# Kernel tuning notes

Hardware: AMD Instinct MI355X
Metric: run time of the kernel (lower is better)

Reference implementation:

```python
import jax, jax.numpy as jnp
import numpy as np

H = 16
D_MODEL = 1024
D_K = D_MODEL // H
NEG = -1e9


def setup_inputs() -> dict:
    key = jax.random.key(0)
    ks = jax.random.split(key, 12)
    B, S = 2, 2048
    inp = {
        "query": jax.random.normal(ks[0], (B, S, D_MODEL), jnp.float32),
        "key": jax.random.normal(ks[1], (B, S, D_MODEL), jnp.float32),
        "value": jax.random.normal(ks[2], (B, S, D_MODEL), jnp.float32),
        "mask": jnp.ones((B, 1, S), jnp.int32),
    }
    s = 1.0 / np.sqrt(D_MODEL)
    for i, nm in enumerate(["Wq", "Wk", "Wv", "Wo"]):
        inp[nm] = jax.random.normal(ks[3 + i], (D_MODEL, D_MODEL), jnp.float32) * s
        inp["b" + nm[1]] = jax.random.normal(ks[7 + i], (D_MODEL,), jnp.float32) * s
    return inp


def _split_heads(x):
    B, S, _ = x.shape
    return x.reshape(B, S, H, D_K).transpose(0, 2, 1, 3)  # [B,H,S,Dk]


def reference(query, key, value, mask, Wq, bq, Wk, bk, Wv, bv, Wo, bo):
    q = _split_heads(query @ Wq + bq)
    k = _split_heads(key @ Wk + bk)
    v = _split_heads(value @ Wv + bv)
    scores = jnp.einsum("bhqd,bhkd->bhqk", q, k) / jnp.sqrt(jnp.float32(D_K))
    # mask [B,1,Sk] -> broadcast as [B,1,1,Sk]
    scores = jnp.where(mask[:, None, :, :] == 0, NEG, scores)
    attn = jax.nn.softmax(scores, axis=-1)  # dropout is identity in eval mode
    out = jnp.einsum("bhqk,bhkd->bhqd", attn, v)
    B, _, Sq, _ = out.shape
    out = out.transpose(0, 2, 1, 3).reshape(B, Sq, H * D_K)
    return out @ Wo + bo
```

## Files before the change

### kernel.cpp

```cpp
#include <hip/hip_runtime.h>
#include <hip/hip_bf16.h>

typedef __attribute__((ext_vector_type(8))) short short8;
typedef __attribute__((ext_vector_type(4))) float float4v;
typedef __hip_bfloat16 bf16;

#define MFMA16(a, b, c) __builtin_amdgcn_mfma_f32_16x16x32_bf16((a), (b), (c), 0, 0, 0)

static __device__ __forceinline__ short8 load8(const bf16* p) {
    return *reinterpret_cast<const short8*>(p);
}
static __device__ __forceinline__ unsigned short bfu(float x) {
    union { bf16 b; unsigned short u; } c; c.b = __float2bfloat16(x); return c.u;
}
static __device__ __forceinline__ unsigned pack2(float lo, float hi) {
    return ((unsigned)bfu(hi) << 16) | bfu(lo);
}
static __device__ __forceinline__ short bf_bits(float x) {
    union { bf16 b; short u; } c; c.b = __float2bfloat16(x); return c.u;
}
static __device__ __forceinline__ short8 cvt8(float4 a, float4 b) {
    short8 r;
    r[0] = bf_bits(a.x); r[1] = bf_bits(a.y); r[2] = bf_bits(a.z); r[3] = bf_bits(a.w);
    r[4] = bf_bits(b.x); r[5] = bf_bits(b.y); r[6] = bf_bits(b.z); r[7] = bf_bits(b.w);
    return r;
}

typedef const __attribute__((address_space(1))) unsigned int* gp1;
typedef __attribute__((address_space(3))) unsigned int* lp3;
static __device__ __forceinline__ void async16(const void* g, void* l) {
    __builtin_amdgcn_global_load_lds((gp1)g, (lp3)l, 16, 0, 0);
}

__global__ __launch_bounds__(256) void transpose_qkv(
    const float* __restrict__ Wq, const float* __restrict__ Wk,
    const float* __restrict__ Wv, bf16* __restrict__ out_base)
{
    __shared__ bf16 tile[64][65];
    const float* in = (blockIdx.z == 0) ? Wq : (blockIdx.z == 1) ? Wk : Wv;
    bf16* out = out_base + (size_t)blockIdx.z * 1048576;
    int tx = threadIdx.x, ty = threadIdx.y;
    int bx = blockIdx.x * 64, by = blockIdx.y * 64;
    for (int i = ty; i < 64; i += 4)
        tile[i][tx] = __float2bfloat16(in[(size_t)(by + i) * 1024 + bx + tx]);
    __syncthreads();
    for (int i = ty; i < 64; i += 4)
        out[(size_t)(bx + i) * 1024 + by + tx] = tile[tx][i];
}

__global__ __launch_bounds__(256) void transpose_one(
    const float* __restrict__ in, bf16* __restrict__ out)
{
    __shared__ bf16 tile[64][65];
    int tx = threadIdx.x, ty = threadIdx.y;
    int bx = blockIdx.x * 64, by = blockIdx.y * 64;
    for (int i = ty; i < 64; i += 4)
        tile[i][tx] = __float2bfloat16(in[(size_t)(by + i) * 1024 + bx + tx]);
    __syncthreads();
    for (int i = ty; i < 64; i += 4)
        out[(size_t)(bx + i) * 1024 + by + tx] = tile[tx][i];
}

__global__ __launch_bounds__(256, 3) void qkv_gemm(
    const float* __restrict__ Xq, const float* __restrict__ Xk,
    const float* __restrict__ Xv, const bf16* __restrict__ Wt_all,
    const float* __restrict__ bq, const float* __restrict__ bk,
    const float* __restrict__ bv,
    bf16* __restrict__ outq, bf16* __restrict__ outk, bf16* __restrict__ outv)
{
    __shared__ float As[2][128 * 32];
    __shared__ bf16  Bs[2][128 * 32];

    int z = blockIdx.z;
    const float* X    = (z == 0) ? Xq : (z == 1) ? Xk : Xv;
    const float* bias = (z == 0) ? bq : (z == 1) ? bk : bv;
    const bf16*  Wt   = Wt_all + (size_t)z * 1048576;
    bf16*        out  = (z == 0) ? outq : (z == 1) ? outk : outv;
    bool vmode = (z == 2);

    int tid = threadIdx.x;
    int w = tid >> 6, lane = tid & 63, l16 = lane & 15, quad = lane >> 4;
    int m_base = blockIdx.y * 128, n_base = blockIdx.x * 128;

    int ra = lane >> 3;
    int sa = (lane & 7) ^ (ra & 7);
    int rb = lane >> 2;
    int sb = (lane & 3) ^ (rb & 3);
    const float* Asrc = X  + (size_t)(m_base + w * 8 + ra) * 1024 + sa * 4;
    const bf16*  Bsrc = Wt + (size_t)(n_base + w * 16 + rb) * 1024 + sb * 8;

    int wm = (w & 1) * 64, wn = (w >> 1) * 64;

    float4v zero = {0.f, 0.f, 0.f, 0.f};
    float4v acc[4][4];
    #pragma unroll
    for (int mi = 0; mi < 4; ++mi)
        #pragma unroll
        for (int nj = 0; nj < 4; ++nj) acc[mi][nj] = zero;

    #pragma unroll
    for (int p = 0; p < 4; ++p)
        async16(Asrc + (size_t)p * 32 * 1024, (char*)As[0] + w * 1024 + p * 4096);
    #pragma unroll
    for (int p = 0; p < 2; ++p)
        async16(Bsrc + (size_t)p * 64 * 1024, (char*)Bs[0] + w * 1024 + p * 4096);
    __syncthreads();

    for (int it = 0; it < 32; ++it) {
        int cur = it & 1, nxt = cur ^ 1;
        int kn = ((it + 1) & 31) * 32;

        #pragma unroll
        for (int p = 0; p < 4; ++p)
            async16(Asrc + (size_t)p * 32 * 1024 + kn,
                    (char*)As[nxt] + w * 1024 + p * 4096);
        #pragma unroll
        for (int p = 0; p < 2; ++p)
            async16(Bsrc + (size_t)p * 64 * 1024 + kn,
                    (char*)Bs[nxt] + w * 1024 + p * 4096);

        short8 af[4], bf[4];
        #pragma unroll
        for (int mi = 0; mi < 4; ++mi) {
            const float* rp = As[cur] + (wm + mi * 16 + l16) * 32;
            float4 f0 = *(const float4*)(rp + (((quad * 2)     ^ (l16 & 7)) << 2));
            float4 f1 = *(const float4*)(rp + (((quad * 2 + 1) ^ (l16 & 7)) << 2));
            af[mi] = cvt8(f0, f1);
        }
        #pragma unroll
        for (int nj = 0; nj < 4; ++nj) {
            const bf16* rp = Bs[cur] + (wn + nj * 16 + l16) * 32;
            bf[nj] = load8(rp + ((quad ^ (l16 & 3)) << 3));
        }
        #pragma unroll
        for (int mi = 0; mi < 4; ++mi)
            #pragma unroll
            for (int nj = 0; nj < 4; ++nj)
                acc[mi][nj] = MFMA16(af[mi], bf[nj], acc[mi][nj]);
        __syncthreads();
    }

    float bsv[4];
    #pragma unroll
    for (int nj = 0; nj < 4; ++nj)
        bsv[nj] = bias[n_base + wn + nj * 16 + l16];

    #pragma unroll
    for (int mi = 0; mi < 4; ++mi) {
        #pragma unroll
        for (int nj = 0; nj < 4; ++nj) {
            int n = n_base + wn + nj * 16 + l16;
            int h = n >> 6, dk = n & 63;
            int m0 = m_base + wm + mi * 16 + quad * 4;
            int b = m0 >> 11, s0 = m0 & 2047;
            if (vmode) {
                float v0 = acc[mi][nj][0] + bsv[nj];
                float v1 = acc[mi][nj][1] + bsv[nj];
                float v2 = acc[mi][nj][2] + bsv[nj];
                float v3 = acc[mi][nj][3] + bsv[nj];
                uint2 pv; pv.x = pack2(v0, v1); pv.y = pack2(v2, v3);
                size_t idx = ((size_t)(b * 16 + h) * 64 + dk) * 2048 + s0;
                *reinterpret_cast<uint2*>(out + idx) = pv;
            } else {
                #pragma unroll
                for (int r = 0; r < 4; ++r) {
                    size_t idx = (((size_t)(b * 16 + h) * 2048 + s0 + r) * 64 + dk);
                    out[idx] = __float2bfloat16(acc[mi][nj][r] + bsv[nj]);
                }
            }
        }
    }
}

__global__ __launch_bounds__(256, 2) void out_gemm(
    const bf16* __restrict__ A, const bf16* __restrict__ Wt,
    const float* __restrict__ bias, float* __restrict__ out)
{
    __shared__ bf16 As[2][128 * 32];
    __shared__ bf16 Bs[2][64 * 32];

    int tid = threadIdx.x;
    int w = tid >> 6, lane = tid & 63, l16 = lane & 15, quad = lane >> 4;
    int m_base = blockIdx.y * 128, n_base = blockIdx.x * 64;

    int rr = lane >> 2;
    int ss = (lane & 3) ^ (rr & 3);
    const bf16* Asrc = A  + (size_t)(m_base + w * 16 + rr) * 1024 + ss * 8;
    const bf16* Bsrc = Wt + (size_t)(n_base + w * 16 + rr) * 1024 + ss * 8;

    int wm = (w & 1) * 64, wn = (w >> 1) * 32;

    float4v zero = {0.f, 0.f, 0.f, 0.f};
    float4v acc[4][2];
    #pragma unroll
    for (int mi = 0; mi < 4; ++mi)
        #pragma unroll
        for (int nj = 0; nj < 2; ++nj) acc[mi][nj] = zero;

    #pragma unroll
    for (int p = 0; p < 2; ++p)
        async16(Asrc + (size_t)p * 64 * 1024, (char*)As[0] + w * 1024 + p * 4096);
    async16(Bsrc, (char*)Bs[0] + w * 1024);
    __syncthreads();

    for (int it = 0; it < 32; ++it) {
        int cur = it & 1, nxt = cur ^ 1;
        int kn = ((it + 1) & 31) * 32;

        #pragma unroll
        for (int p = 0; p < 2; ++p)
            async16(Asrc + (size_t)p * 64 * 1024 + kn,
                    (char*)As[nxt] + w * 1024 + p * 4096);
        async16(Bsrc + kn, (char*)Bs[nxt] + w * 1024);

        short8 af[4], bf[2];
        #pragma unroll
        for (int mi = 0; mi < 4; ++mi) {
            const bf16* rp = As[cur] + (wm + mi * 16 + l16) * 32;
            af[mi] = load8(rp + ((quad ^ (l16 & 3)) << 3));
        }
        #pragma unroll
        for (int nj = 0; nj < 2; ++nj) {
            const bf16* rp = Bs[cur] + (wn + nj * 16 + l16) * 32;
            bf[nj] = load8(rp + ((quad ^ (l16 & 3)) << 3));
        }
        #pragma unroll
        for (int mi = 0; mi < 4; ++mi)
            #pragma unroll
            for (int nj = 0; nj < 2; ++nj)
                acc[mi][nj] = MFMA16(af[mi], bf[nj], acc[mi][nj]);
        __syncthreads();
    }

    float bsv[2];
    #pragma unroll
    for (int nj = 0; nj < 2; ++nj)
        bsv[nj] = bias[n_base + wn + nj * 16 + l16];

    #pragma unroll
    for (int mi = 0; mi < 4; ++mi)
        #pragma unroll
        for (int nj = 0; nj < 2; ++nj) {
            int n = n_base + wn + nj * 16 + l16;
            int m0 = m_base + wm + mi * 16 + quad * 4;
            #pragma unroll
            for (int r = 0; r < 4; ++r)
                out[(size_t)(m0 + r) * 1024 + n] = acc[mi][nj][r] + bsv[nj];
        }
}

__global__ __launch_bounds__(256, 2) void attn_fused(
    const bf16* __restrict__ Qm, const bf16* __restrict__ Km,
    const bf16* __restrict__ Vt, const int* __restrict__ mask,
    bf16* __restrict__ Oout)
{
    __shared__ float biasL[2048];
    __shared__ __align__(16) bf16 Kc[2][64 * 64];
    __shared__ __align__(16) bf16 Vc[2][64 * 64];
    __shared__ __align__(16) bf16 P[4][32 * 72];

    int tid = threadIdx.x;
    int w = tid >> 6, lane = tid & 63, l16 = lane & 15, quad = lane >> 4;
    int bh = blockIdx.x >> 4, qg = blockIdx.x & 15;
    int b = bh >> 4, h = bh & 15;
    int tile0 = (qg * 4 + w) * 2;

    const int* mb = mask + b * 2048;
    for (int i = tid; i < 2048; i += 256)
        biasL[i] = (mb[i] == 0) ? -2.0e9f : 0.0f;

    short8 bQ[2][2];
    #pragma unroll
    for (int qi = 0; qi < 2; ++qi) {
        const bf16* Qb = Qm + ((size_t)bh * 2048 + (size_t)(tile0 + qi) * 16) * 64;
        bQ[qi][0] = load8(Qb + l16 * 64 + quad * 8);
        bQ[qi][1] = load8(Qb + l16 * 64 + 32 + quad * 8);
    }

    int r8 = lane >> 3;
    int sl = (lane & 7) ^ (r8 & 7);
    const bf16* Kb = Km + (size_t)bh * 2048 * 64;
    const bf16* Vb = Vt + (size_t)bh * 64 * 2048;
    const bf16* Ksrc = Kb + (size_t)(w * 8 + r8) * 64 + sl * 8;
    const bf16* Vsrc = Vb + (size_t)(w * 8 + r8) * 2048 + sl * 8;

    bf16* Pw = &P[w][0];
    int sw = l16 & 7;

    float4v zero = {0.f, 0.f, 0.f, 0.f};
    float4v Oacc[2][4];
    #pragma unroll
    for (int qi = 0; qi < 2; ++qi)
        #pragma unroll
        for (int g = 0; g < 4; ++g) Oacc[qi][g] = zero;
    float lsum[2] = {0.f, 0.f};
    const float C = 0.18033688f;

    async16(Ksrc, (char*)Kc[0] + w * 1024);
    async16(Ksrc + (size_t)32 * 64, (char*)Kc[0] + w * 1024 + 4096);
    async16(Vsrc, (char*)Vc[0] + w * 1024);
    async16(Vsrc + (size_t)32 * 2048, (char*)Vc[0] + w * 1024 + 4096);
    __syncthreads();

    for (int it = 0; it < 32; ++it) {
        int cur = it & 1, nxt = cur ^ 1;
        int kt = it * 64;
        int kn = ((it + 1) & 31) * 64;

        async16(Ksrc + (size_t)kn * 64, (char*)Kc[nxt] + w * 1024);
        async16(Ksrc + (size_t)(kn + 32) * 64, (char*)Kc[nxt] + w * 1024 + 4096);
        async16(Vsrc + kn, (char*)Vc[nxt] + w * 1024);
        async16(Vsrc + (size_t)32 * 2048 + kn, (char*)Vc[nxt] + w * 1024 + 4096);

        float4v S[2][4];
        #pragma unroll
        for (int kj = 0; kj < 4; ++kj) {
            const bf16* kr = Kc[cur] + (kj * 16 + l16) * 64;
            short8 a0 = load8(kr + (((0 + quad) ^ sw) << 3));
            short8 a1 = load8(kr + (((4 + quad) ^ sw) << 3));
            #pragma unroll
            for (int qi = 0; qi < 2; ++qi) {
                float4v s = zero;
                s = MFMA16(a0, bQ[qi][0], s);
                s = MFMA16(a1, bQ[qi][1], s);
                S[qi][kj] = s;
            }
        }

        #pragma unroll
        for (int kj = 0; kj < 4; ++kj) {
            float4 bv4 = *reinterpret_cast<const float4*>(&biasL[kt + kj * 16 + quad * 4]);
            const float* bb = reinterpret_cast<const float*>(&bv4);
            #pragma unroll
            for (int qi = 0; qi < 2; ++qi) {
                float p[4];
                #pragma unroll
                for (int r = 0; r < 4; ++r)
                    p[r] = __builtin_amdgcn_exp2f(fmaf(S[qi][kj][r], C, bb[r]));
                lsum[qi] += (p[0] + p[1]) + (p[2] + p[3]);
                uint2 pw; pw.x = pack2(p[0], p[1]); pw.y = pack2(p[2], p[3]);
                *reinterpret_cast<uint2*>(
                    &Pw[(qi * 16 + l16) * 72 + kj * 16 + quad * 4]) = pw;
            }
        }

        short8 ap[2][2];
        #pragma unroll
        for (int qi = 0; qi < 2; ++qi) {
            ap[qi][0] = load8(&Pw[(qi * 16 + l16) * 72 + quad * 8]);
            ap[qi][1] = load8(&Pw[(qi * 16 + l16) * 72 + 32 + quad * 8]);
        }
        #pragma unroll
        for (int g = 0; g < 4; ++g) {
            const bf16* vr = Vc[cur] + (g * 16 + l16) * 64;
            short8 v0 = load8(vr + (((0 + quad) ^ sw) << 3));
            short8 v1 = load8(vr + (((4 + quad) ^ sw) << 3));
            #pragma unroll
            for (int qi = 0; qi < 2; ++qi) {
                Oacc[qi][g] = MFMA16(ap[qi][0], v0, Oacc[qi][g]);
                Oacc[qi][g] = MFMA16(ap[qi][1], v1, Oacc[qi][g]);
            }
        }
        __syncthreads();
    }

    #pragma unroll
    for (int qi = 0; qi < 2; ++qi) {
        float ls = lsum[qi];
        ls += __shfl_xor(ls, 16, 64);
        ls += __shfl_xor(ls, 32, 64);
        #pragma unroll
        for (int r = 0; r < 4; ++r) {
            float linv = 1.f / __shfl(ls, quad * 4 + r, 64);
            int srow = (tile0 + qi) * 16 + quad * 4 + r;
            size_t base = ((size_t)b * 2048 + srow) * 1024 + h * 64;
            #pragma unroll
            for (int g = 0; g < 4; ++g)
                Oout[base + g * 16 + l16] = __float2bfloat16(Oacc[qi][g][r] * linv);
        }
    }
}

extern "C" void kernel_launch(void* const* d_in, const int* in_sizes, int n_in,
                              void* d_out, int out_size, void* d_ws, size_t ws_size,
                              hipStream_t stream) {
    const float* query = (const float*)d_in[0];
    const float* key   = (const float*)d_in[1];
    const float* value = (const float*)d_in[2];
    const int*   mask  = (const int*)d_in[3];
    const float* Wq = (const float*)d_in[4];
    const float* bq = (const float*)d_in[5];
    const float* Wk = (const float*)d_in[6];
    const float* bk = (const float*)d_in[7];
    const float* Wv = (const float*)d_in[8];
    const float* bv = (const float*)d_in[9];
    const float* Wo = (const float*)d_in[10];
    const float* bo = (const float*)d_in[11];

    char* ws = (char*)d_ws;
    const size_t MB = 1024 * 1024;
    bf16* vb     = (bf16*)ws;
    bf16* Wt_all = (bf16*)(ws + 8 * MB);
    bf16* aout   = (bf16*)(ws + 8 * MB);
    bf16* WtO    = (bf16*)ws;
    bf16* qb     = (bf16*)d_out;
    bf16* kb     = (bf16*)((char*)d_out + 8 * MB);
    float* out   = (float*)d_out;

    transpose_qkv<<<dim3(16, 16, 3), dim3(64, 4), 0, stream>>>(Wq, Wk, Wv, Wt_all);

    qkv_gemm<<<dim3(8, 32, 3), 256, 0, stream>>>(
        query, key, value, Wt_all, bq, bk, bv, qb, kb, vb);

    attn_fused<<<dim3(512), dim3(256), 0, stream>>>(qb, kb, vb, mask, aout);

    transpose_one<<<dim3(16, 16), dim3(64, 4), 0, stream>>>(Wo, WtO);

    out_gemm<<<dim3(16, 32), 256, 0, stream>>>(aout, WtO, bo, out);
}
```

Baseline: 271.2 us.

## Remap blocks per XCD, bit-pack mask, single-buffer K/V for higher attention occupancy

Block indices for the QKV GEMM, the output GEMM and attention are remapped so blocks that share operands (same head, same M rows) land on the same XCD and can reuse its L2. In attention the float bias array is replaced by a 64-bit ballot mask, with a fast path that skips masking when a whole chunk is unmasked. K/V double buffering is dropped to shrink LDS so four blocks can fit per CU. The cost is that loads are no longer prefetched, so each iteration waits on its own K/V fetch at a barrier.

Result: no change. 274.2 us (+1.1%).

```diff
diff --git a/kernel.cpp b/kernel.cpp
--- a/kernel.cpp
+++ b/kernel.cpp
@@ -71,7 +71,14 @@
     __shared__ float As[2][128 * 32];
     __shared__ bf16  Bs[2][128 * 32];
 
-    int z = blockIdx.z;
+    int wg = blockIdx.x;
+    int xcd = wg & 7;
+    int jj = wg >> 3;
+    int grp = xcd * 12 + (jj >> 3);
+    int z = grp >> 5;
+    int m_blk = grp & 31;
+    int n_blk = jj & 7;
+
     const float* X    = (z == 0) ? Xq : (z == 1) ? Xk : Xv;
     const float* bias = (z == 0) ? bq : (z == 1) ? bk : bv;
     const bf16*  Wt   = Wt_all + (size_t)z * 1048576;
@@ -80,7 +87,7 @@
 
     int tid = threadIdx.x;
     int w = tid >> 6, lane = tid & 63, l16 = lane & 15, quad = lane >> 4;
-    int m_base = blockIdx.y * 128, n_base = blockIdx.x * 128;
+    int m_base = m_blk * 128, n_base = n_blk * 128;
 
     int ra = lane >> 3;
     int sa = (lane & 7) ^ (ra & 7);
@@ -179,9 +186,15 @@
     __shared__ bf16 As[2][128 * 32];
     __shared__ bf16 Bs[2][64 * 32];
 
+    int wg = blockIdx.x;
+    int xcd = wg & 7;
+    int jj = wg >> 3;
+    int m_blk = xcd * 4 + (jj >> 4);
+    int n_blk = jj & 15;
+
     int tid = threadIdx.x;
     int w = tid >> 6, lane = tid & 63, l16 = lane & 15, quad = lane >> 4;
-    int m_base = blockIdx.y * 128, n_base = blockIdx.x * 64;
+    int m_base = m_blk * 128, n_base = n_blk * 64;
 
     int rr = lane >> 2;
     int ss = (lane & 3) ^ (rr & 3);
@@ -249,25 +262,32 @@
         }
 }
 
-__global__ __launch_bounds__(256, 2) void attn_fused(
+__global__ __launch_bounds__(256, 4) void attn_fused(
     const bf16* __restrict__ Qm, const bf16* __restrict__ Km,
     const bf16* __restrict__ Vt, const int* __restrict__ mask,
     bf16* __restrict__ Oout)
 {
-    __shared__ float biasL[2048];
-    __shared__ __align__(16) bf16 Kc[2][64 * 64];
-    __shared__ __align__(16) bf16 Vc[2][64 * 64];
+    __shared__ __align__(16) bf16 Kc[64 * 64];
+    __shared__ __align__(16) bf16 Vc[64 * 64];
     __shared__ __align__(16) bf16 P[4][32 * 72];
+    __shared__ unsigned long long maskb[32];
 
     int tid = threadIdx.x;
     int w = tid >> 6, lane = tid & 63, l16 = lane & 15, quad = lane >> 4;
-    int bh = blockIdx.x >> 4, qg = blockIdx.x & 15;
+    int wg = blockIdx.x;
+    int xcd = wg & 7;
+    int jj = wg >> 3;
+    int bh = xcd * 4 + (jj >> 4);
+    int qg = jj & 15;
     int b = bh >> 4, h = bh & 15;
     int tile0 = (qg * 4 + w) * 2;
 
     const int* mb = mask + b * 2048;
-    for (int i = tid; i < 2048; i += 256)
-        biasL[i] = (mb[i] == 0) ? -2.0e9f : 0.0f;
+    #pragma unroll
+    for (int i = 0; i < 8; ++i) {
+        unsigned long long bal = __ballot(mb[w * 512 + i * 64 + lane] != 0);
+        if (lane == 0) maskb[w * 8 + i] = bal;
+    }
 
     short8 bQ[2][2];
     #pragma unroll
@@ -279,10 +299,10 @@
 
     int r8 = lane >> 3;
     int sl = (lane & 7) ^ (r8 & 7);
-    const bf16* Kb = Km + (size_t)bh * 2048 * 64;
-    const bf16* Vb = Vt + (size_t)bh * 64 * 2048;
-    const bf16* Ksrc = Kb + (size_t)(w * 8 + r8) * 64 + sl * 8;
-    const bf16* Vsrc = Vb + (size_t)(w * 8 + r8) * 2048 + sl * 8;
+    const bf16* Ksrc = Km + (size_t)bh * 2048 * 64 + (size_t)(w * 8 + r8) * 64 + sl * 8;
+    const bf16* Vsrc = Vt + (size_t)bh * 64 * 2048 + (size_t)(w * 8 + r8) * 2048 + sl * 8;
+    char* Kdst = (char*)Kc + w * 1024;
+    char* Vdst = (char*)Vc + w * 1024;
 
     bf16* Pw = &P[w][0];
     int sw = l16 & 7;
@@ -296,26 +316,21 @@
     float lsum[2] = {0.f, 0.f};
     const float C = 0.18033688f;
 
-    async16(Ksrc, (char*)Kc[0] + w * 1024);
-    async16(Ksrc + (size_t)32 * 64, (char*)Kc[0] + w * 1024 + 4096);
-    async16(Vsrc, (char*)Vc[0] + w * 1024);
-    async16(Vsrc + (size_t)32 * 2048, (char*)Vc[0] + w * 1024 + 4096);
-    __syncthreads();
-
     for (int it = 0; it < 32; ++it) {
-        int cur = it & 1, nxt = cur ^ 1;
         int kt = it * 64;
-        int kn = ((it + 1) & 31) * 64;
-
-        async16(Ksrc + (size_t)kn * 64, (char*)Kc[nxt] + w * 1024);
-        async16(Ksrc + (size_t)(kn + 32) * 64, (char*)Kc[nxt] + w * 1024 + 4096);
-        async16(Vsrc + kn, (char*)Vc[nxt] + w * 1024);
-        async16(Vsrc + (size_t)32 * 2048 + kn, (char*)Vc[nxt] + w * 1024 + 4096);
+        async16(Ksrc + (size_t)kt * 64, Kdst);
+        async16(Ksrc + (size_t)(kt + 32) * 64, Kdst + 4096);
+        async16(Vsrc + kt, Vdst);
+        async16(Vsrc + (size_t)32 * 2048 + kt, Vdst + 4096);
+        __syncthreads();
+
+        unsigned long long m64 = maskb[it];
+        bool full = (m64 == ~0ull);
 
         float4v S[2][4];
         #pragma unroll
         for (int kj = 0; kj < 4; ++kj) {
-            const bf16* kr = Kc[cur] + (kj * 16 + l16) * 64;
+            const bf16* kr = Kc + (kj * 16 + l16) * 64;
             short8 a0 = load8(kr + (((0 + quad) ^ sw) << 3));
             short8 a1 = load8(kr + (((4 + quad) ^ sw) << 3));
             #pragma unroll
@@ -329,14 +344,18 @@
 
         #pragma unroll
         for (int kj = 0; kj < 4; ++kj) {
-            float4 bv4 = *reinterpret_cast<const float4*>(&biasL[kt + kj * 16 + quad * 4]);
-            const float* bb = reinterpret_cast<const float*>(&bv4);
+            unsigned m4 = (unsigned)(m64 >> (kj * 16 + quad * 4)) & 0xFu;
             #pragma unroll
             for (int qi = 0; qi < 2; ++qi) {
                 float p[4];
                 #pragma unroll
                 for (int r = 0; r < 4; ++r)
-                    p[r] = __builtin_amdgcn_exp2f(fmaf(S[qi][kj][r], C, bb[r]));
+                    p[r] = __builtin_amdgcn_exp2f(S[qi][kj][r] * C);
+                if (!full) {
+                    #pragma unroll
+                    for (int r = 0; r < 4; ++r)
+                        p[r] = ((m4 >> r) & 1u) ? p[r] : 0.f;
+                }
                 lsum[qi] += (p[0] + p[1]) + (p[2] + p[3]);
                 uint2 pw; pw.x = pack2(p[0], p[1]); pw.y = pack2(p[2], p[3]);
                 *reinterpret_cast<uint2*>(
@@ -352,7 +371,7 @@
         }
         #pragma unroll
         for (int g = 0; g < 4; ++g) {
-            const bf16* vr = Vc[cur] + (g * 16 + l16) * 64;
+            const bf16* vr = Vc + (g * 16 + l16) * 64;
             short8 v0 = load8(vr + (((0 + quad) ^ sw) << 3));
             short8 v1 = load8(vr + (((4 + quad) ^ sw) << 3));
             #pragma unroll
@@ -409,12 +428,12 @@
 
     transpose_qkv<<<dim3(16, 16, 3), dim3(64, 4), 0, stream>>>(Wq, Wk, Wv, Wt_all);
 
-    qkv_gemm<<<dim3(8, 32, 3), 256, 0, stream>>>(
+    qkv_gemm<<<dim3(768), 256, 0, stream>>>(
         query, key, value, Wt_all, bq, bk, bv, qb, kb, vb);
 
-    attn_fused<<<dim3(512), dim3(256), 0, stream>>>(qb, kb, vb, mask, aout);
+    attn_fused<<<dim3(512), 256, 0, stream>>>(qb, kb, vb, mask, aout);
 
     transpose_one<<<dim3(16, 16), dim3(64, 4), 0, stream>>>(Wo, WtO);
 
-    out_gemm<<<dim3(16, 32), 256, 0, stream>>>(aout, WtO, bo, out);
-}
+    out_gemm<<<dim3(512), 256, 0, stream>>>(aout, WtO, bo, out);
+}
```
